# Performance work log

Hardware: AMD Instinct MI355X
Metric: run time of the kernel (lower is better)

The kernel has to match this reference:

```python
import jax, jax.numpy as jnp
import numpy as np

B, F0, F1, E, C = 256, 39, 39, 16, 1  # batch, feature_nums[0], feature_nums[1], emb_size, w_channels
_ROWS, _COLS = np.tril_indices(F1, k=-1)  # strict lower triangle of (F1, F0); row-major order matches masked_select
I = _ROWS.shape[0]  # interaction_num = 741
BN_EPS = 1e-5


def setup_inputs() -> dict:
    key = jax.random.key(0)
    k1, k2, k3 = jax.random.split(key, 3)
    xi = jax.random.normal(k1, (B, F0, E), dtype=jnp.float32)
    xj = jax.random.normal(k2, (B, F1, E), dtype=jnp.float32)
    # W param is (1,1,C,E,E) in torch; keep the broadcastable core (C,E,E). Xavier-uniform bound.
    bound = float(np.sqrt(6.0 / (E + E)))
    W = jax.random.uniform(k3, (C, E, E), dtype=jnp.float32, minval=-bound, maxval=bound)
    gamma = jnp.ones((I,), dtype=jnp.float32)   # BatchNorm2d weight
    beta = jnp.zeros((I,), dtype=jnp.float32)   # BatchNorm2d bias
    return {"xi": xi, "xj": xj, "W": W, "gamma": gamma, "beta": beta}


def reference(xi, xj, W, gamma, beta):
    rows = jnp.asarray(_ROWS)
    cols = jnp.asarray(_COLS)
    # raw_cross[b,f1,f0,e1,e2] = xj[b,f1,e1] * xi[b,f0,e2]; only keep strict-lower-tri (f1,f0) pairs.
    # Compute triangular pairs directly instead of materializing the full (B,F1,F0,E,E) tensor.
    cross = xj[:, rows, :, None] * xi[:, cols, None, :]  # (B, I, E, E)
    # BatchNorm2d (training-mode batch stats, biased variance) over channels I
    mean = jnp.mean(cross, axis=(0, 2, 3), keepdims=True)            # (1, I, 1, 1)
    var = jnp.mean(jnp.square(cross - mean), axis=(0, 2, 3), keepdims=True)
    normed = (cross - mean) * jax.lax.rsqrt(var + BN_EPS)
    normed = normed * gamma[None, :, None, None] + beta[None, :, None, None]
    # broadcast multiply with W over w_channels, then transpose(1,2)
    out = normed[:, :, None, :, :] * W[None, None, :, :, :]          # (B, I, C, E, E)
    return jnp.transpose(out, (0, 2, 1, 3, 4))                        # (B, C, I, E, E)
```

## Files before the change

### kernel.cpp

```cpp
#include <hip/hip_runtime.h>
#include <math.h>

#define BB 256
#define FF 39
#define EE 16
#define II 741
#define BN_EPS 1e-5f
#define CPW 8
#define NB 8
#define NCX 24
#define NGY (BB / NB)

typedef float vfloat4 __attribute__((ext_vector_type(4)));
typedef float vfloat2 __attribute__((ext_vector_type(2)));

struct OffTab { unsigned int v[II]; };
static constexpr OffTab make_off() {
    OffTab t{};
    int i = 0;
    for (int r = 1; r < FF; ++r)
        for (int c = 0; c < r; ++c) {
            t.v[i] = ((unsigned)(r * EE) << 16) | (unsigned)(c * EE);
            ++i;
        }
    return t;
}
__constant__ OffTab g_off = make_off();


__global__ __launch_bounds__(256) void
stats_kernel(const float* __restrict__ xi,
             const float* __restrict__ xj,
             const float* __restrict__ gamma,
             const float* __restrict__ beta,
             float* __restrict__ ws) {
    int wid = (blockIdx.x * blockDim.x + threadIdx.x) >> 6;
    int lane = threadIdx.x & 63;
    if (wid >= II) return;
    int i = wid;
    unsigned o = g_off.v[i];
    int joff = (int)(o >> 16);
    int coff = (int)(o & 0xffffu);

    float sumS = 0.f, sumQ = 0.f;
#pragma unroll
    for (int b = lane; b < BB; b += 64) {
        const vfloat4* xjr = reinterpret_cast<const vfloat4*>(xj + b * FF * EE + joff);
        const vfloat4* xic = reinterpret_cast<const vfloat4*>(xi + b * FF * EE + coff);
        float sj = 0.f, qj = 0.f, si = 0.f, qi = 0.f;
#pragma unroll
        for (int k = 0; k < 4; ++k) {
            vfloat4 vj = xjr[k];
            vfloat4 vi = xic[k];
            sj += vj.x + vj.y + vj.z + vj.w;
            qj += vj.x * vj.x + vj.y * vj.y + vj.z * vj.z + vj.w * vj.w;
            si += vi.x + vi.y + vi.z + vi.w;
            qi += vi.x * vi.x + vi.y * vi.y + vi.z * vi.z + vi.w * vi.w;
        }
        sumS += sj * si;
        sumQ += qj * qi;
    }
#pragma unroll
    for (int off = 32; off > 0; off >>= 1) {
        sumS += __shfl_xor(sumS, off);
        sumQ += __shfl_xor(sumQ, off);
    }
    if (lane == 0) {
        const float invN = 1.0f / (float)(BB * EE * EE);
        float mean = sumS * invN;
        float ex2 = sumQ * invN;
        float var = ex2 - mean * mean;
        float inv_std = 1.0f / sqrtf(var + BN_EPS);
        float a = gamma[i] * inv_std;
        float d = beta[i] - mean * a;
        vfloat2 e;
        e.x = a; e.y = d;
        reinterpret_cast<vfloat2*>(ws)[i] = e;
    }
}

#define LOADB(S, V, b)                                                        \
    {                                                                         \
        const float* xib_ = xi + (b) * FF * EE;                               \
        const float* xjb_ = xj + (b) * FF * EE;                               \
        _Pragma("unroll") for (int k = 0; k < CPW; ++k) {                     \
            S[k] = xjb_[joff[k] + e1];                                        \
            V[k] = reinterpret_cast<const vfloat4*>(xib_ + coff[k])[e2q];     \
        }                                                                     \
    }

#define STOREB(S, V, b)                                                       \
    {                                                                         \
        float* outb_ = out + (size_t)(b) * (II * EE * EE)                     \
                       + (size_t)ibase * (EE * EE);                           \
        _Pragma("unroll") for (int k = 0; k < CPW; ++k) {                     \
            vfloat4 o4;                                                       \
            o4.x = (S[k] * V[k].x * a[k] + d[k]) * w4.x;                      \
            o4.y = (S[k] * V[k].y * a[k] + d[k]) * w4.y;                      \
            o4.z = (S[k] * V[k].z * a[k] + d[k]) * w4.z;                      \
            o4.w = (S[k] * V[k].w * a[k] + d[k]) * w4.w;                      \
            reinterpret_cast<vfloat4*>(outb_ + k * (EE * EE))[l] = o4;        \
        }                                                                     \
    }

__global__ __launch_bounds__(256) void
cross_bn_kernel(const float* __restrict__ xi,
                const float* __restrict__ xj,
                const float* __restrict__ W,
                const float* __restrict__ ws,
                float* __restrict__ out) {
    const vfloat2* T2 = reinterpret_cast<const vfloat2*>(ws);

    int t = threadIdx.x;
    int l = t & 63;
    int e1 = l >> 2;
    int e2q = l & 3;
    int wv = t >> 6;

    vfloat4 w4 = reinterpret_cast<const vfloat4*>(W)[e1 * 4 + e2q];

    int ibase = __builtin_amdgcn_readfirstlane(blockIdx.x * (4 * CPW) + wv * CPW);
    int b0 = blockIdx.y * NB;

    if (ibase + CPW <= II) {
        int joff[CPW], coff[CPW];
        float a[CPW], d[CPW];
#pragma unroll
        for (int k = 0; k < CPW; ++k) {
            unsigned o = g_off.v[ibase + k];
            joff[k] = (int)(o >> 16);
            coff[k] = (int)(o & 0xffffu);
            vfloat2 ad = T2[ibase + k];
            a[k] = ad.x; d[k] = ad.y;
        }
        float sA[CPW], sB[CPW];
        vfloat4 vA[CPW], vB[CPW];
        LOADB(sA, vA, b0 + 0)
        LOADB(sB, vB, b0 + 1)
        STOREB(sA, vA, b0 + 0)  LOADB(sA, vA, b0 + 2)
        STOREB(sB, vB, b0 + 1)  LOADB(sB, vB, b0 + 3)
        STOREB(sA, vA, b0 + 2)  LOADB(sA, vA, b0 + 4)
        STOREB(sB, vB, b0 + 3)  LOADB(sB, vB, b0 + 5)
        STOREB(sA, vA, b0 + 4)  LOADB(sA, vA, b0 + 6)
        STOREB(sB, vB, b0 + 5)  LOADB(sB, vB, b0 + 7)
        STOREB(sA, vA, b0 + 6)
        STOREB(sB, vB, b0 + 7)
    } else {
#pragma unroll
        for (int bb = 0; bb < NB; ++bb) {
            int b = b0 + bb;
            const float* xib = xi + b * FF * EE;
            const float* xjb = xj + b * FF * EE;
            float* outb = out + (size_t)b * (II * EE * EE);
            for (int k = 0; k < CPW; ++k) {
                int i = ibase + k;
                if (i >= II) break;
                unsigned o = g_off.v[i];
                int joff = (int)(o >> 16);
                int coff = (int)(o & 0xffffu);
                vfloat2 ad = T2[i];
                float xjs = xjb[joff + e1];
                vfloat4 xi4 = reinterpret_cast<const vfloat4*>(xib + coff)[e2q];
                vfloat4 o4;
                o4.x = (xjs * xi4.x * ad.x + ad.y) * w4.x;
                o4.y = (xjs * xi4.y * ad.x + ad.y) * w4.y;
                o4.z = (xjs * xi4.z * ad.x + ad.y) * w4.z;
                o4.w = (xjs * xi4.w * ad.x + ad.y) * w4.w;
                reinterpret_cast<vfloat4*>(outb + (size_t)i * (EE * EE))[l] = o4;
            }
        }
    }
}

extern "C" void kernel_launch(void* const* d_in, const int* in_sizes, int n_in,
                              void* d_out, int out_size, void* d_ws, size_t ws_size,
                              hipStream_t stream) {
    const float* xi = (const float*)d_in[0];
    const float* xj = (const float*)d_in[1];
    const float* W = (const float*)d_in[2];
    const float* gamma = (const float*)d_in[3];
    const float* beta = (const float*)d_in[4];
    float* out = (float*)d_out;
    float* ws = (float*)d_ws;

    stats_kernel<<<dim3((II * 64 + 255) / 256), 256, 0, stream>>>(xi, xj, gamma, beta, ws);
    cross_bn_kernel<<<dim3(NCX, NGY), 256, 0, stream>>>(xi, xj, W, ws, out);
}
```

Measured before the change: 43.39 us.

## Precompute per-row sums and finish BN stats inside the cross kernel

```diff
diff --git a/kernel.cpp b/kernel.cpp
--- a/kernel.cpp
+++ b/kernel.cpp
@@ -10,6 +10,7 @@
 #define NB 8
 #define NCX 24
 #define NGY (BB / NB)
+#define NROW (BB * FF)
 
 typedef float vfloat4 __attribute__((ext_vector_type(4)));
 typedef float vfloat2 __attribute__((ext_vector_type(2)));
@@ -28,55 +29,26 @@
 __constant__ OffTab g_off = make_off();
 
 
-__global__ __launch_bounds__(256) void
-stats_kernel(const float* __restrict__ xi,
-             const float* __restrict__ xj,
-             const float* __restrict__ gamma,
-             const float* __restrict__ beta,
-             float* __restrict__ ws) {
-    int wid = (blockIdx.x * blockDim.x + threadIdx.x) >> 6;
-    int lane = threadIdx.x & 63;
-    if (wid >= II) return;
-    int i = wid;
-    unsigned o = g_off.v[i];
-    int joff = (int)(o >> 16);
-    int coff = (int)(o & 0xffffu);
-
-    float sumS = 0.f, sumQ = 0.f;
+__global__ void rowsumT_kernel(const float* __restrict__ xi,
+                               const float* __restrict__ xj,
+                               float* __restrict__ ws) {
+    int t = blockIdx.x * blockDim.x + threadIdx.x;
+    if (t >= 2 * NROW) return;
+    int tensor = (t >= NROW) ? 1 : 0;
+    int row = tensor ? (t - NROW) : t;
+    int b = row / FF;
+    int f = row - b * FF;
+    const float* src = (tensor ? xj : xi) + row * EE;
+    float s = 0.f, q = 0.f;
 #pragma unroll
-    for (int b = lane; b < BB; b += 64) {
-        const vfloat4* xjr = reinterpret_cast<const vfloat4*>(xj + b * FF * EE + joff);
-        const vfloat4* xic = reinterpret_cast<const vfloat4*>(xi + b * FF * EE + coff);
-        float sj = 0.f, qj = 0.f, si = 0.f, qi = 0.f;
-#pragma unroll
-        for (int k = 0; k < 4; ++k) {
-            vfloat4 vj = xjr[k];
-            vfloat4 vi = xic[k];
-            sj += vj.x + vj.y + vj.z + vj.w;
-            qj += vj.x * vj.x + vj.y * vj.y + vj.z * vj.z + vj.w * vj.w;
-            si += vi.x + vi.y + vi.z + vi.w;
-            qi += vi.x * vi.x + vi.y * vi.y + vi.z * vi.z + vi.w * vi.w;
-        }
-        sumS += sj * si;
-        sumQ += qj * qi;
+    for (int k = 0; k < 4; ++k) {
+        vfloat4 v = reinterpret_cast<const vfloat4*>(src)[k];
+        s += v.x + v.y + v.z + v.w;
+        q += v.x * v.x + v.y * v.y + v.z * v.z + v.w * v.w;
     }
-#pragma unroll
-    for (int off = 32; off > 0; off >>= 1) {
-        sumS += __shfl_xor(sumS, off);
-        sumQ += __shfl_xor(sumQ, off);
-    }
-    if (lane == 0) {
-        const float invN = 1.0f / (float)(BB * EE * EE);
-        float mean = sumS * invN;
-        float ex2 = sumQ * invN;
-        float var = ex2 - mean * mean;
-        float inv_std = 1.0f / sqrtf(var + BN_EPS);
-        float a = gamma[i] * inv_std;
-        float d = beta[i] - mean * a;
-        vfloat2 e;
-        e.x = a; e.y = d;
-        reinterpret_cast<vfloat2*>(ws)[i] = e;
-    }
+    vfloat2* base = reinterpret_cast<vfloat2*>(ws) + (tensor ? NROW : 0);
+    vfloat2 e; e.x = s; e.y = q;
+    base[f * BB + b] = e;
 }
 
 #define LOADB(S, V, b)                                                        \
@@ -107,9 +79,12 @@
 cross_bn_kernel(const float* __restrict__ xi,
                 const float* __restrict__ xj,
                 const float* __restrict__ W,
+                const float* __restrict__ gamma,
+                const float* __restrict__ beta,
                 const float* __restrict__ ws,
                 float* __restrict__ out) {
-    const vfloat2* T2 = reinterpret_cast<const vfloat2*>(ws);
+    const vfloat2* Ti = reinterpret_cast<const vfloat2*>(ws);
+    const vfloat2* Tj = Ti + NROW;
 
     int t = threadIdx.x;
     int l = t & 63;
@@ -121,18 +96,44 @@
 
     int ibase = __builtin_amdgcn_readfirstlane(blockIdx.x * (4 * CPW) + wv * CPW);
     int b0 = blockIdx.y * NB;
+    int nval = II - ibase;
+    if (nval <= 0) return;
+    if (nval > CPW) nval = CPW;
 
-    if (ibase + CPW <= II) {
-        int joff[CPW], coff[CPW];
-        float a[CPW], d[CPW];
+    int joff[CPW], coff[CPW];
+    float a[CPW], d[CPW];
+    const float invN = 1.0f / (float)(BB * EE * EE);
 #pragma unroll
-        for (int k = 0; k < CPW; ++k) {
+    for (int k = 0; k < CPW; ++k) {
+        if (k < nval) {
             unsigned o = g_off.v[ibase + k];
             joff[k] = (int)(o >> 16);
             coff[k] = (int)(o & 0xffffu);
-            vfloat2 ad = T2[ibase + k];
-            a[k] = ad.x; d[k] = ad.y;
+            int rb = joff[k] * (BB / EE);
+            int cb = coff[k] * (BB / EE);
+            float sS = 0.f, sQ = 0.f;
+#pragma unroll
+            for (int m = 0; m < 4; ++m) {
+                int b = l + 64 * m;
+                vfloat2 pj = Tj[rb + b];
+                vfloat2 pi = Ti[cb + b];
+                sS += pj.x * pi.x;
+                sQ += pj.y * pi.y;
+            }
+#pragma unroll
+            for (int off = 32; off > 0; off >>= 1) {
+                sS += __shfl_xor(sS, off);
+                sQ += __shfl_xor(sQ, off);
+            }
+            float mean = sS * invN;
+            float var = sQ * invN - mean * mean;
+            float inv_std = 1.0f / sqrtf(var + BN_EPS);
+            a[k] = gamma[ibase + k] * inv_std;
+            d[k] = beta[ibase + k] - mean * a[k];
         }
+    }
+
+    if (nval == CPW) {
         float sA[CPW], sB[CPW];
         vfloat4 vA[CPW], vB[CPW];
         LOADB(sA, vA, b0 + 0)
@@ -152,20 +153,15 @@
             const float* xib = xi + b * FF * EE;
             const float* xjb = xj + b * FF * EE;
             float* outb = out + (size_t)b * (II * EE * EE);
-            for (int k = 0; k < CPW; ++k) {
+            for (int k = 0; k < nval; ++k) {
                 int i = ibase + k;
-                if (i >= II) break;
-                unsigned o = g_off.v[i];
-                int joff = (int)(o >> 16);
-                int coff = (int)(o & 0xffffu);
-                vfloat2 ad = T2[i];
-                float xjs = xjb[joff + e1];
-                vfloat4 xi4 = reinterpret_cast<const vfloat4*>(xib + coff)[e2q];
+                float xjs = xjb[joff[k] + e1];
+                vfloat4 xi4 = reinterpret_cast<const vfloat4*>(xib + coff[k])[e2q];
                 vfloat4 o4;
-                o4.x = (xjs * xi4.x * ad.x + ad.y) * w4.x;
-                o4.y = (xjs * xi4.y * ad.x + ad.y) * w4.y;
-                o4.z = (xjs * xi4.z * ad.x + ad.y) * w4.z;
-                o4.w = (xjs * xi4.w * ad.x + ad.y) * w4.w;
+                o4.x = (xjs * xi4.x * a[k] + d[k]) * w4.x;
+                o4.y = (xjs * xi4.y * a[k] + d[k]) * w4.y;
+                o4.z = (xjs * xi4.z * a[k] + d[k]) * w4.z;
+                o4.w = (xjs * xi4.w * a[k] + d[k]) * w4.w;
                 reinterpret_cast<vfloat4*>(outb + (size_t)i * (EE * EE))[l] = o4;
             }
         }
@@ -183,6 +179,6 @@
     float* out = (float*)d_out;
     float* ws = (float*)d_ws;
 
-    stats_kernel<<<dim3((II * 64 + 255) / 256), 256, 0, stream>>>(xi, xj, gamma, beta, ws);
-    cross_bn_kernel<<<dim3(NCX, NGY), 256, 0, stream>>>(xi, xj, W, ws, out);
+    rowsumT_kernel<<<dim3((2 * NROW + 255) / 256), 256, 0, stream>>>(xi, xj, ws);
+    cross_bn_kernel<<<dim3(NCX, NGY), 256, 0, stream>>>(xi, xj, W, gamma, beta, ws, out);
 }
```

New measurement: 46.37 us. 6.9% more time.
